# Kernel optimization log

Measured on AMD Instinct MI355X. Metric: run time of the kernel, lower is better.

Reference implementation:

```python
import jax, jax.numpy as jnp
import numpy as np

BN_EPS = 1e-5


def grid_sample_bilinear(img, grid):
    """Torch F.grid_sample, mode=bilinear, padding_mode=zeros, align_corners=False.
    img: (B, C, H, W); grid: (B, N, 2) in [-1, 1] -> (B, C, N)."""
    B, C, H, W = img.shape
    x = ((grid[..., 0] + 1.0) * W - 1.0) * 0.5  # (B, N) pixel coords
    y = ((grid[..., 1] + 1.0) * H - 1.0) * 0.5
    x0 = jnp.floor(x)
    y0 = jnp.floor(y)
    x1 = x0 + 1.0
    y1 = y0 + 1.0
    wx1 = x - x0
    wx0 = 1.0 - wx1
    wy1 = y - y0
    wy0 = 1.0 - wy1
    img_flat = img.reshape(B, C, H * W)

    def corner(xi, yi, w):
        valid = (xi >= 0) & (xi <= W - 1) & (yi >= 0) & (yi <= H - 1)
        xi_c = jnp.clip(xi, 0, W - 1).astype(jnp.int32)
        yi_c = jnp.clip(yi, 0, H - 1).astype(jnp.int32)
        idx = yi_c * W + xi_c  # (B, N)
        vals = jnp.take_along_axis(img_flat, idx[:, None, :], axis=2)  # (B, C, N)
        return vals * (w * valid.astype(img.dtype))[:, None, :]

    return (corner(x0, y0, wx0 * wy0) + corner(x1, y0, wx1 * wy0)
            + corner(x0, y1, wx0 * wy1) + corner(x1, y1, wx1 * wy1))


def conv1x1(x, w, b):
    # x: (B, Cin, N), w: (Cout, Cin), b: (Cout,)
    return jnp.einsum('oi,bin->bon', w, x) + b[None, :, None]


def batchnorm1d_train(x, gamma, beta):
    # training-mode BN over (batch, length) per channel, biased variance
    mean = jnp.mean(x, axis=(0, 2), keepdims=True)
    var = jnp.mean((x - mean) ** 2, axis=(0, 2), keepdims=True)
    xn = (x - mean) * jax.lax.rsqrt(var + BN_EPS)
    return xn * gamma[None, :, None] + beta[None, :, None]


def setup_inputs() -> dict:
    key = jax.random.key(0)
    ks = jax.random.split(key, 12)
    B, N, CI, CP, H, W, R = 4, 16384, 256, 256, 64, 160, 4
    Cin = CI + CP
    Cb = CP // R

    def glorot(k, shape):
        fan_in = shape[1]
        return jax.random.normal(k, shape, dtype=jnp.float32) * (1.0 / np.sqrt(fan_in))

    return {
        'pts_img': jax.random.uniform(ks[0], (B, N, 2), dtype=jnp.float32, minval=-1.0, maxval=1.0),
        'img_feats': jax.random.normal(ks[1], (B, CI, H, W), dtype=jnp.float32),
        'pts_feats': jax.random.normal(ks[2], (B, CP, N), dtype=jnp.float32),
        'fusion_w': glorot(ks[3], (CP, Cin)),
        'fusion_b': jax.random.normal(ks[4], (CP,), dtype=jnp.float32) * 0.01,
        'bn_gamma': jnp.ones((CP,), dtype=jnp.float32),
        'bn_beta': jnp.zeros((CP,), dtype=jnp.float32),
        'ca1_w': glorot(ks[5], (Cb, CP)),
        'ca1_b': jax.random.normal(ks[6], (Cb,), dtype=jnp.float32) * 0.01,
        'ca2_w': glorot(ks[7], (CP, Cb)),
        'ca2_b': jax.random.normal(ks[8], (CP,), dtype=jnp.float32) * 0.01,
        'sa_w': glorot(ks[9], (Cb, CP)),
        'sa_b': jax.random.normal(ks[10], (Cb,), dtype=jnp.float32) * 0.01,
    }


def reference(pts_img, img_feats, pts_feats, fusion_w, fusion_b, bn_gamma, bn_beta,
              ca1_w, ca1_b, ca2_w, ca2_b, sa_w, sa_b):
    # grid_sample gather: (B, C_I, N)
    pts_wise_img_feats = grid_sample_bilinear(img_feats, pts_img)
    fusion = jnp.concatenate([pts_wise_img_feats, pts_feats], axis=1)  # (B, C_I+C_P, N)
    # fusion MLP: conv1x1 + BN + ReLU
    fusion = jax.nn.relu(batchnorm1d_train(conv1x1(fusion, fusion_w, fusion_b), bn_gamma, bn_beta))
    # spatial attention: max over channels of bottleneck conv, sigmoid gate
    spatial = jax.nn.sigmoid(jnp.max(conv1x1(fusion, sa_w, sa_b), axis=1, keepdims=True))
    fusion = spatial * fusion
    # channel attention: bottleneck MLP, global max-pool over points, sigmoid gate
    ca = conv1x1(jax.nn.relu(conv1x1(fusion, ca1_w, ca1_b)), ca2_w, ca2_b)  # (B, C_P, N)
    channel = jax.nn.sigmoid(jnp.max(ca, axis=2, keepdims=True))  # (B, C_P, 1)
    return channel * fusion
```

## Files before the change

### kernel.cpp

```cpp
#include <hip/hip_runtime.h>
#include <stdint.h>


typedef __attribute__((ext_vector_type(8))) short bf16x8;
typedef __attribute__((ext_vector_type(4))) float f32x4;

#define B_ 4
#define N_ 16384
#define H_ 64
#define W_ 160
#define HW_ (H_ * W_)
#define K_ 512

__device__ __forceinline__ float bf2f(unsigned short u) {
    union { unsigned int i; float f; } c; c.i = ((unsigned int)u) << 16; return c.f;
}
__device__ __forceinline__ unsigned short f2bf(float f) {
    union { float f; unsigned int i; } c; c.f = f;
    unsigned int u = c.i;
    return (unsigned short)((u + 0x7FFFu + ((u >> 16) & 1u)) >> 16);
}
__device__ __forceinline__ unsigned int fkey(float f) {
    union { float f; unsigned int u; int i; } c; c.f = f;
    return (c.i < 0) ? ~c.u : (c.u | 0x80000000u);
}
__device__ __forceinline__ float funkey(unsigned int k) {
    union { unsigned int u; float f; } c;
    c.u = (k & 0x80000000u) ? (k & 0x7FFFFFFFu) : ~k;
    return c.f;
}

__device__ __forceinline__ void async_copy16(void* lds, const void* g) {
#if defined(__has_builtin) && __has_builtin(__builtin_amdgcn_global_load_lds)
    __builtin_amdgcn_global_load_lds(
        (const __attribute__((address_space(1))) unsigned int*)g,
        (__attribute__((address_space(3))) unsigned int*)lds, 16, 0, 0);
#else
    *(uint4*)lds = *(const uint4*)g;
#endif
}

__global__ __launch_bounds__(256) void k_imgt(const float* __restrict__ img,
                                              unsigned short* __restrict__ imgT,
                                              const float* __restrict__ fw,
                                              const float* __restrict__ saw,
                                              const float* __restrict__ c1w,
                                              const float* __restrict__ c2w,
                                              unsigned short* WfB, unsigned short* saB,
                                              unsigned short* ca1B, unsigned short* ca2B,
                                              float* buckets, unsigned int* camax) {
    int t = threadIdx.x;
    int bx = blockIdx.x;
    if (bx < 2560) {
        __shared__ __align__(16) unsigned short tile[64 * 68];
        int hw0 = (bx % 160) * 64, c0 = ((bx / 160) & 3) * 64, b = bx / 640;
        const float* src = img + ((size_t)b * 256 + c0) * HW_ + hw0;
        int sub = (t & 15) * 4, grp = t >> 4;
#pragma unroll
        for (int it = 0; it < 4; ++it) {
            int cl = grp + it * 16;
            float4 v = *(const float4*)(src + (size_t)cl * HW_ + sub);
            ushort4 o;
            o.x = f2bf(v.x); o.y = f2bf(v.y); o.z = f2bf(v.z); o.w = f2bf(v.w);
            *(ushort4*)(tile + cl * 68 + sub) = o;
        }
        __syncthreads();
        unsigned short* dst = imgT + ((size_t)b * HW_ + hw0) * 256 + c0;
#pragma unroll
        for (int it = 0; it < 4; ++it) {
            int hwl = grp + it * 16;
            ushort4 o;
            o.x = tile[(sub + 0) * 68 + hwl];
            o.y = tile[(sub + 1) * 68 + hwl];
            o.z = tile[(sub + 2) * 68 + hwl];
            o.w = tile[(sub + 3) * 68 + hwl];
            *(ushort4*)(dst + (size_t)hwl * 256 + sub) = o;
        }
    } else {
        int j = bx - 2560;
        if (j == 0) {
            for (int i = t; i < 16 * 512; i += 256) buckets[i] = 0.f;
            for (int i = t; i < 8 * 1024; i += 256) camax[i] = 0u;
        }
        int i = j * 256 + t;
        if (i < 131072) WfB[i] = f2bf(fw[i]);
        else if (i < 147456) saB[i - 131072] = f2bf(saw[i - 131072]);
        else if (i < 163840) ca1B[i - 147456] = f2bf(c1w[i - 147456]);
        else if (i < 180224) ca2B[i - 163840] = f2bf(c2w[i - 163840]);
    }
}

__global__ __launch_bounds__(256, 3) void k_gemm1f(const unsigned short* __restrict__ WfB,
                                                   const float* __restrict__ pim,
                                                   const unsigned short* __restrict__ imgT,
                                                   const float* __restrict__ pts,
                                                   const float* __restrict__ fb,
                                                   unsigned short* __restrict__ Y,
                                                   float* __restrict__ buckets) {
    __shared__ __align__(16) char smem[47104];
    unsigned short* At = (unsigned short*)smem;
    unsigned short* Bt = (unsigned short*)(smem + 32768);
    unsigned short* tile = (unsigned short*)smem;
    uint4*  offs4 = (uint4*)(smem + 41984);
    float4* wts4  = (float4*)(smem + 43008);
    float* biasS  = (float*)(smem + 44032);
    float* redS   = (float*)(smem + 45056);
    float* redQ   = (float*)(smem + 46080);

    int t = threadIdx.x;
    int n0 = blockIdx.x * 64, bb = blockIdx.y;
    int w = t >> 6, lane = t & 63, quad = lane >> 4, l15 = lane & 15;
    const unsigned short* imb = imgT + (size_t)bb * HW_ * 256;

    if (t < 64) {
        float2 g2 = *(const float2*)(pim + (size_t)((size_t)bb * N_ + n0 + t) * 2);
        float x = (g2.x + 1.0f) * (0.5f * W_) - 0.5f;
        float y = (g2.y + 1.0f) * (0.5f * H_) - 0.5f;
        float xf = floorf(x), yf = floorf(y);
        float wx1 = x - xf, wx0 = 1.0f - wx1;
        float wy1 = y - yf, wy0 = 1.0f - wy1;
        int x0 = (int)xf, y0 = (int)yf;
        int x1 = x0 + 1, y1 = y0 + 1;
        float vx0 = (x0 >= 0 && x0 < W_) ? 1.f : 0.f;
        float vx1 = (x1 >= 0 && x1 < W_) ? 1.f : 0.f;
        float vy0 = (y0 >= 0 && y0 < H_) ? 1.f : 0.f;
        float vy1 = (y1 >= 0 && y1 < H_) ? 1.f : 0.f;
        int cx0 = min(max(x0, 0), W_ - 1), cx1 = min(max(x1, 0), W_ - 1);
        int cy0 = min(max(y0, 0), H_ - 1), cy1 = min(max(y1, 0), H_ - 1);
        uint4 o4;
        o4.x = (unsigned)(cy0 * W_ + cx0);
        o4.y = (unsigned)(cy0 * W_ + cx1);
        o4.z = (unsigned)(cy1 * W_ + cx0);
        o4.w = (unsigned)(cy1 * W_ + cx1);
        offs4[t] = o4;
        float4 w4;
        w4.x = wx0 * wy0 * vx0 * vy0;
        w4.y = wx1 * wy0 * vx1 * vy0;
        w4.z = wx0 * wy1 * vx0 * vy1;
        w4.w = wx1 * wy1 * vx1 * vy1;
        wts4[t] = w4;
    }
    biasS[t] = fb[t];

    int arow_lo = t >> 3;
    int aslot = (t & 7) ^ ((t >> 3) & 7);

    const f32x4 fzero = {0.f, 0.f, 0.f, 0.f};
    f32x4 acc[4][4];
#pragma unroll
    for (int i = 0; i < 4; ++i)
#pragma unroll
        for (int j = 0; j < 4; ++j) acc[i][j] = fzero;

    for (int kt = 0; kt < 8; ++kt) {
        int k0 = kt * 64;
        __syncthreads();
#pragma unroll
        for (int q = 0; q < 8; ++q) {
            int row = q * 32 + arow_lo;
            async_copy16(At + (size_t)q * 2048 + (size_t)t * 8,
                         WfB + (size_t)row * K_ + k0 + aslot * 8);
        }
        if (kt < 4) {
#pragma unroll
            for (int pass = 0; pass < 2; ++pass) {
                int tau = pass * 256 + t;
                int pt = tau >> 3, cg = tau & 7;
                uint4 o4 = offs4[pt];
                float4 w4 = wts4[pt];
                int ch = k0 + cg * 8;
                uint4 cA = *(const uint4*)(imb + (size_t)o4.x * 256 + ch);
                uint4 cB = *(const uint4*)(imb + (size_t)o4.y * 256 + ch);
                uint4 cC = *(const uint4*)(imb + (size_t)o4.z * 256 + ch);
                uint4 cD = *(const uint4*)(imb + (size_t)o4.w * 256 + ch);
                const unsigned short* pa = (const unsigned short*)&cA;
                const unsigned short* pb = (const unsigned short*)&cB;
                const unsigned short* pc = (const unsigned short*)&cC;
                const unsigned short* pd = (const unsigned short*)&cD;
                uint4 ov;
                unsigned short* po = (unsigned short*)&ov;
#pragma unroll
                for (int e = 0; e < 8; ++e)
                    po[e] = f2bf(w4.x * bf2f(pa[e]) + w4.y * bf2f(pb[e]) +
                                 w4.z * bf2f(pc[e]) + w4.w * bf2f(pd[e]));
                *(uint4*)(Bt + pt * 72 + cg * 8) = ov;
            }
        } else {
            int c_local = t & 63, g = t >> 6;
            int c = (kt - 4) * 64 + c_local;
            const float* src = pts + ((size_t)bb * 256 + c) * (size_t)N_ + n0 + g * 16;
            float4 v0 = *(const float4*)(src + 0);
            float4 v1 = *(const float4*)(src + 4);
            float4 v2 = *(const float4*)(src + 8);
            float4 v3 = *(const float4*)(src + 12);
            unsigned short* dst = Bt + (size_t)(g * 16) * 72 + c_local;
            dst[0 * 72] = f2bf(v0.x); dst[1 * 72] = f2bf(v0.y);
            dst[2 * 72] = f2bf(v0.z); dst[3 * 72] = f2bf(v0.w);
            dst[4 * 72] = f2bf(v1.x); dst[5 * 72] = f2bf(v1.y);
            dst[6 * 72] = f2bf(v1.z); dst[7 * 72] = f2bf(v1.w);
            dst[8 * 72] = f2bf(v2.x); dst[9 * 72] = f2bf(v2.y);
            dst[10 * 72] = f2bf(v2.z); dst[11 * 72] = f2bf(v2.w);
            dst[12 * 72] = f2bf(v3.x); dst[13 * 72] = f2bf(v3.y);
            dst[14 * 72] = f2bf(v3.z); dst[15 * 72] = f2bf(v3.w);
        }
        __syncthreads();
#pragma unroll
        for (int kk = 0; kk < 2; ++kk) {
            bf16x8 af[4], bv[4];
#pragma unroll
            for (int j = 0; j < 4; ++j)
                bv[j] = *(const bf16x8*)(Bt + (j * 16 + l15) * 72 + kk * 32 + quad * 8);
#pragma unroll
            for (int i = 0; i < 4; ++i) {
                int mloc = w * 64 + i * 16 + l15;
                int slot = (kk * 4 + quad) ^ (l15 & 7);
                af[i] = *(const bf16x8*)(At + (size_t)mloc * 64 + slot * 8);
            }
#pragma unroll
            for (int i = 0; i < 4; ++i)
#pragma unroll
                for (int j = 0; j < 4; ++j)
                    acc[i][j] = __builtin_amdgcn_mfma_f32_16x16x32_bf16(af[i], bv[j], acc[i][j], 0, 0, 0);
        }
    }

    __syncthreads();
#pragma unroll
    for (int i = 0; i < 4; ++i) {
        int mloc = w * 64 + i * 16 + quad * 4;
        float b0 = biasS[mloc + 0], b1 = biasS[mloc + 1];
        float b2 = biasS[mloc + 2], b3 = biasS[mloc + 3];
        float s0 = 0.f, q0 = 0.f, s1 = 0.f, q1 = 0.f;
        float s2 = 0.f, q2 = 0.f, s3 = 0.f, q3 = 0.f;
#pragma unroll
        for (int j = 0; j < 4; ++j) {
            int n = j * 16 + l15;
            float y0 = acc[i][j][0] + b0;
            float y1 = acc[i][j][1] + b1;
            float y2 = acc[i][j][2] + b2;
            float y3 = acc[i][j][3] + b3;
            s0 += y0; q0 += y0 * y0;
            s1 += y1; q1 += y1 * y1;
            s2 += y2; q2 += y2 * y2;
            s3 += y3; q3 += y3 * y3;
            ushort4 o;
            o.x = f2bf(y0); o.y = f2bf(y1); o.z = f2bf(y2); o.w = f2bf(y3);
            *(ushort4*)(tile + n * 264 + mloc) = o;
        }
#pragma unroll
        for (int d = 1; d < 16; d <<= 1) {
            s0 += __shfl_xor(s0, d, 64); q0 += __shfl_xor(q0, d, 64);
            s1 += __shfl_xor(s1, d, 64); q1 += __shfl_xor(q1, d, 64);
            s2 += __shfl_xor(s2, d, 64); q2 += __shfl_xor(q2, d, 64);
            s3 += __shfl_xor(s3, d, 64); q3 += __shfl_xor(q3, d, 64);
        }
        if (l15 == 0) {
            redS[mloc + 0] = s0; redQ[mloc + 0] = q0;
            redS[mloc + 1] = s1; redQ[mloc + 1] = q1;
            redS[mloc + 2] = s2; redQ[mloc + 2] = q2;
            redS[mloc + 3] = s3; redQ[mloc + 3] = q3;
        }
    }
    __syncthreads();
    {
        float* bk = buckets + (size_t)(blockIdx.x & 15) * 512;
        atomicAdd(bk + t, redS[t]);
        atomicAdd(bk + 256 + t, redQ[t]);
    }
    size_t Yrow0 = ((size_t)bb * N_ + n0) * 256;
#pragma unroll
    for (int pass = 0; pass < 8; ++pass) {
        int row = pass * 8 + (t >> 5);
        int col = (t & 31) * 8;
        *(uint4*)(Y + Yrow0 + (size_t)row * 256 + col) = *(const uint4*)(tile + row * 264 + col);
    }
}

__global__ __launch_bounds__(256, 2) void k_gate(const unsigned short* __restrict__ Y,
                                                 const float* __restrict__ buckets,
                                                 const float* __restrict__ gamma,
                                                 const float* __restrict__ beta,
                                                 const unsigned short* __restrict__ saB,
                                                 const float* __restrict__ sab,
                                                 const unsigned short* __restrict__ c1B,
                                                 const float* __restrict__ c1b,
                                                 const unsigned short* __restrict__ c2B,
                                                 unsigned int* __restrict__ camax,
                                                 float* __restrict__ sp_g,
                                                 float* __restrict__ ss_out) {
    __shared__ __align__(16) unsigned short Ft[64 * 264];
    __shared__ __align__(16) unsigned short Ht[64 * 72];
    __shared__ float scS[256], shS[256];
    __shared__ float saPart[4][64];
    __shared__ float spL[64];
    int t = threadIdx.x;
    size_t pts0 = (size_t)blockIdx.x * 64;
    int b = (int)(pts0 >> 14);
    int w = t >> 6, lane = t & 63, quad = lane >> 4, l15 = lane & 15;
    int jrow = w * 16 + l15;

    bf16x8 bvs[8], bvc[8];
#pragma unroll
    for (int kt = 0; kt < 8; ++kt) {
        bvs[kt] = *(const bf16x8*)(saB + (size_t)jrow * 256 + kt * 32 + quad * 8);
        bvc[kt] = *(const bf16x8*)(c1B + (size_t)jrow * 256 + kt * 32 + quad * 8);
    }
    float sbias = sab[jrow];
    float cbias = c1b[jrow];

    {
        float s = 0.f, q = 0.f;
#pragma unroll
        for (int bk = 0; bk < 16; ++bk) {
            s += buckets[bk * 512 + t];
            q += buckets[bk * 512 + 256 + t];
        }
        const float inv = 1.0f / (float)(B_ * N_);
        float mean = s * inv;
        float var = q * inv - mean * mean;
        float sc = gamma[t] * rsqrtf(var + 1e-5f);
        float sh = beta[t] - mean * sc;
        scS[t] = sc;
        shS[t] = sh;
        if (blockIdx.x == 0) { ss_out[t] = sc; ss_out[256 + t] = sh; }
    }
    __syncthreads();

    int cc = (t * 8) & 255;
    float scr[8], shr[8];
#pragma unroll
    for (int e = 0; e < 8; ++e) { scr[e] = scS[cc + e]; shr[e] = shS[cc + e]; }
    for (int idx = t * 8; idx < 64 * 256; idx += 2048) {
        int r = idx >> 8;
        uint4 v = *(const uint4*)(Y + (pts0 + r) * 256 + cc);
        unsigned short* us = (unsigned short*)&v;
#pragma unroll
        for (int e = 0; e < 8; ++e) {
            float f = bf2f(us[e]) * scr[e] + shr[e];
            us[e] = f2bf(fmaxf(f, 0.f));
        }
        *(uint4*)(Ft + r * 264 + cc) = v;
    }
    __syncthreads();

    const f32x4 fzero = {0.f, 0.f, 0.f, 0.f};
    f32x4 accS[4], accC[4];
#pragma unroll
    for (int i = 0; i < 4; ++i) { accS[i] = fzero; accC[i] = fzero; }
#pragma unroll
    for (int kt = 0; kt < 8; ++kt) {
        bf16x8 af[4];
#pragma unroll
        for (int i = 0; i < 4; ++i)
            af[i] = *(const bf16x8*)(Ft + (i * 16 + l15) * 264 + kt * 32 + quad * 8);
#pragma unroll
        for (int i = 0; i < 4; ++i) {
            accS[i] = __builtin_amdgcn_mfma_f32_16x16x32_bf16(af[i], bvs[kt], accS[i], 0, 0, 0);
            accC[i] = __builtin_amdgcn_mfma_f32_16x16x32_bf16(af[i], bvc[kt], accC[i], 0, 0, 0);
        }
    }
#pragma unroll
    for (int i = 0; i < 4; ++i) {
#pragma unroll
        for (int r = 0; r < 4; ++r) {
            float v = accS[i][r] + sbias;
#pragma unroll
            for (int d = 1; d < 16; d <<= 1) v = fmaxf(v, __shfl_xor(v, d, 64));
            if (l15 == 0) saPart[w][i * 16 + quad * 4 + r] = v;
        }
    }
    __syncthreads();
    if (t < 64) {
        float m4 = fmaxf(fmaxf(saPart[0][t], saPart[1][t]),
                         fmaxf(saPart[2][t], saPart[3][t]));
        float sv = 1.0f / (1.0f + __expf(-m4));
        spL[t] = sv;
        sp_g[pts0 + t] = sv;
    }
    __syncthreads();

#pragma unroll
    for (int i = 0; i < 4; ++i) {
#pragma unroll
        for (int r = 0; r < 4; ++r) {
            int pt = i * 16 + quad * 4 + r;
            float hv = fmaxf(accC[i][r] * spL[pt] + cbias, 0.f);
            Ht[pt * 72 + jrow] = f2bf(hv);
        }
    }
    __syncthreads();

    {
        bf16x8 b2a[4], b2b[4];
#pragma unroll
        for (int mt = 0; mt < 4; ++mt) {
            b2a[mt] = *(const bf16x8*)(c2B + (size_t)(w * 64 + mt * 16 + l15) * 64 + quad * 8);
            b2b[mt] = *(const bf16x8*)(c2B + (size_t)(w * 64 + mt * 16 + l15) * 64 + 32 + quad * 8);
        }
        float vmax[4] = {-3e38f, -3e38f, -3e38f, -3e38f};
#pragma unroll
        for (int i = 0; i < 4; ++i) {
            bf16x8 a0 = *(const bf16x8*)(Ht + (i * 16 + l15) * 72 + quad * 8);
            bf16x8 a1 = *(const bf16x8*)(Ht + (i * 16 + l15) * 72 + 32 + quad * 8);
#pragma unroll
            for (int mt = 0; mt < 4; ++mt) {
                f32x4 acc = __builtin_amdgcn_mfma_f32_16x16x32_bf16(a0, b2a[mt], fzero, 0, 0, 0);
                acc = __builtin_amdgcn_mfma_f32_16x16x32_bf16(a1, b2b[mt], acc, 0, 0, 0);
#pragma unroll
                for (int r = 0; r < 4; ++r) vmax[mt] = fmaxf(vmax[mt], acc[r]);
            }
        }
        unsigned int* cam = camax + (size_t)(blockIdx.x & 7) * 1024 + b * 256;
#pragma unroll
        for (int mt = 0; mt < 4; ++mt) {
            float v = vmax[mt];
            v = fmaxf(v, __shfl_xor(v, 16, 64));
            v = fmaxf(v, __shfl_xor(v, 32, 64));
            if (quad == 0) atomicMax(cam + w * 64 + mt * 16 + l15, fkey(v));
        }
    }
}

__global__ __launch_bounds__(256) void k_out(const unsigned short* __restrict__ Y,
                                             const unsigned int* __restrict__ camax,
                                             const float* __restrict__ c2b,
                                             const float* __restrict__ ss,
                                             const float* __restrict__ sp_g,
                                             float* __restrict__ out) {
    __shared__ __align__(16) unsigned short tile[64 * 68];
    __shared__ float ch[64], scT[64], shT[64], spT[64];
    int t = threadIdx.x;
    int n0 = blockIdx.x * 64, m0 = blockIdx.y * 64, b = blockIdx.z;
    if (t < 64) {
        int m = m0 + t;
        unsigned int k = 0u;
#pragma unroll
        for (int bk = 0; bk < 8; ++bk) k = max(k, camax[bk * 1024 + b * 256 + m]);
        ch[t] = 1.0f / (1.0f + __expf(-(funkey(k) + c2b[m])));
        scT[t] = ss[m];
        shT[t] = ss[256 + m];
        spT[t] = sp_g[(size_t)b * N_ + n0 + t];
    }
    int sub = (t & 15) * 4, grp = t >> 4;
    const unsigned short* src = Y + ((size_t)b * N_ + n0) * 256 + m0;
#pragma unroll
    for (int it = 0; it < 4; ++it) {
        int nl = grp + it * 16;
        ushort4 v = *(const ushort4*)(src + (size_t)nl * 256 + sub);
        *(ushort4*)(tile + nl * 68 + sub) = v;
    }
    __syncthreads();
    float* dst = out + ((size_t)b * 256 + m0) * N_ + n0;
#pragma unroll
    for (int it = 0; it < 4; ++it) {
        int ml = grp + it * 16;
        float g = ch[ml], scv = scT[ml], shv = shT[ml];
        float4 o;
        o.x = fmaxf(bf2f(tile[(sub + 0) * 68 + ml]) * scv + shv, 0.f) * spT[sub + 0] * g;
        o.y = fmaxf(bf2f(tile[(sub + 1) * 68 + ml]) * scv + shv, 0.f) * spT[sub + 1] * g;
        o.z = fmaxf(bf2f(tile[(sub + 2) * 68 + ml]) * scv + shv, 0.f) * spT[sub + 2] * g;
        o.w = fmaxf(bf2f(tile[(sub + 3) * 68 + ml]) * scv + shv, 0.f) * spT[sub + 3] * g;
        *(float4*)(dst + (size_t)ml * N_ + sub) = o;
    }
}

extern "C" void kernel_launch(void* const* d_in, const int* in_sizes, int n_in,
                              void* d_out, int out_size, void* d_ws, size_t ws_size,
                              hipStream_t stream) {
    (void)in_sizes; (void)n_in; (void)out_size; (void)ws_size;
    const float* pts_img = (const float*)d_in[0];
    const float* img     = (const float*)d_in[1];
    const float* pts     = (const float*)d_in[2];
    const float* fw      = (const float*)d_in[3];
    const float* fbias   = (const float*)d_in[4];
    const float* gamma   = (const float*)d_in[5];
    const float* beta    = (const float*)d_in[6];
    const float* c1w     = (const float*)d_in[7];
    const float* c1b     = (const float*)d_in[8];
    const float* c2w     = (const float*)d_in[9];
    const float* c2b     = (const float*)d_in[10];
    const float* saw     = (const float*)d_in[11];
    const float* sab     = (const float*)d_in[12];
    float* out = (float*)d_out;

    char* ws = (char*)d_ws;
    unsigned short* imgT = (unsigned short*)(ws);
    unsigned short* Y    = (unsigned short*)(ws + 20971520);
    unsigned short* WfB  = (unsigned short*)(ws + 54525952);
    unsigned short* saB  = (unsigned short*)(ws + 54788096);
    unsigned short* ca1B = (unsigned short*)(ws + 54820864);
    unsigned short* ca2B = (unsigned short*)(ws + 54853632);
    float* buckets       = (float*)(ws + 54886400);
    unsigned int* camax  = (unsigned int*)(ws + 54919168);
    float* sp_g          = (float*)(ws + 54951936);
    float* ss            = (float*)(ws + 55214080);

    k_imgt<<<3264, 256, 0, stream>>>(img, imgT, fw, saw, c1w, c2w,
                                     WfB, saB, ca1B, ca2B, buckets, camax);
    k_gemm1f<<<dim3(256, 4), 256, 0, stream>>>(WfB, pts_img, imgT, pts, fbias, Y, buckets);
    k_gate<<<1024, 256, 0, stream>>>(Y, buckets, gamma, beta, saB, sab, ca1B, c1b,
                                     ca2B, camax, sp_g, ss);
    k_out<<<dim3(256, 4, 4), 256, 0, stream>>>(Y, camax, c2b, ss, sp_g, out);
}
```

Baseline: 250.0 us.

## Widen k_out tiles to all channels, interleave gemm1 batches, raise gate occupancy

k_out now has each block load a full 64-point by 256-channel Y tile with 16-byte row-contiguous reads and write all 256 channels, replacing 64x64 sub-tiles. The scale, shift and channel-gate setup therefore runs once per block rather than once per channel group, and the grid shrinks from 4096 to 1024 blocks. k_gemm1f switches to a 1D grid with the batch index in the low bits, so consecutive blocks cover different batches and spread their gathers and atomic buckets. k_gate's launch bounds go from 2 to 3 blocks per SM, which may force register spills. The larger k_out tile uses about 35KB of LDS, which limits how many blocks can be resident per CU.

```diff
diff --git a/kernel.cpp b/kernel.cpp
--- a/kernel.cpp
+++ b/kernel.cpp
@@ -108,7 +108,9 @@
     float* redQ   = (float*)(smem + 46080);
 
     int t = threadIdx.x;
-    int n0 = blockIdx.x * 64, bb = blockIdx.y;
+    int bid = blockIdx.x;
+    int bb = bid & 3;
+    int n0 = (bid >> 2) * 64;
     int w = t >> 6, lane = t & 63, quad = lane >> 4, l15 = lane & 15;
     const unsigned short* imb = imgT + (size_t)bb * HW_ * 256;
 
@@ -263,7 +265,7 @@
     }
     __syncthreads();
     {
-        float* bk = buckets + (size_t)(blockIdx.x & 15) * 512;
+        float* bk = buckets + (size_t)(bid & 15) * 512;
         atomicAdd(bk + t, redS[t]);
         atomicAdd(bk + 256 + t, redQ[t]);
     }
@@ -276,7 +278,7 @@
     }
 }
 
-__global__ __launch_bounds__(256, 2) void k_gate(const unsigned short* __restrict__ Y,
+__global__ __launch_bounds__(256, 3) void k_gate(const unsigned short* __restrict__ Y,
                                                  const float* __restrict__ buckets,
                                                  const float* __restrict__ gamma,
                                                  const float* __restrict__ beta,
@@ -427,40 +429,40 @@
                                              const float* __restrict__ ss,
                                              const float* __restrict__ sp_g,
                                              float* __restrict__ out) {
-    __shared__ __align__(16) unsigned short tile[64 * 68];
-    __shared__ float ch[64], scT[64], shT[64], spT[64];
+    __shared__ __align__(16) unsigned short tile[64 * 264];
+    __shared__ float ch[256], scT[256], shT[256], spT[64];
     int t = threadIdx.x;
-    int n0 = blockIdx.x * 64, m0 = blockIdx.y * 64, b = blockIdx.z;
-    if (t < 64) {
-        int m = m0 + t;
+    int n0 = blockIdx.x * 64, b = blockIdx.y;
+    {
+        int m = t;
         unsigned int k = 0u;
 #pragma unroll
         for (int bk = 0; bk < 8; ++bk) k = max(k, camax[bk * 1024 + b * 256 + m]);
         ch[t] = 1.0f / (1.0f + __expf(-(funkey(k) + c2b[m])));
         scT[t] = ss[m];
         shT[t] = ss[256 + m];
-        spT[t] = sp_g[(size_t)b * N_ + n0 + t];
-    }
+    }
+    if (t < 64) spT[t] = sp_g[(size_t)b * N_ + n0 + t];
+    const unsigned short* src = Y + ((size_t)b * N_ + n0) * 256;
+#pragma unroll
+    for (int pass = 0; pass < 8; ++pass) {
+        int row = pass * 8 + (t >> 5);
+        int col = (t & 31) * 8;
+        *(uint4*)(tile + row * 264 + col) = *(const uint4*)(src + (size_t)row * 256 + col);
+    }
+    __syncthreads();
     int sub = (t & 15) * 4, grp = t >> 4;
-    const unsigned short* src = Y + ((size_t)b * N_ + n0) * 256 + m0;
-#pragma unroll
-    for (int it = 0; it < 4; ++it) {
-        int nl = grp + it * 16;
-        ushort4 v = *(const ushort4*)(src + (size_t)nl * 256 + sub);
-        *(ushort4*)(tile + nl * 68 + sub) = v;
-    }
-    __syncthreads();
-    float* dst = out + ((size_t)b * 256 + m0) * N_ + n0;
-#pragma unroll
-    for (int it = 0; it < 4; ++it) {
+#pragma unroll
+    for (int it = 0; it < 16; ++it) {
         int ml = grp + it * 16;
         float g = ch[ml], scv = scT[ml], shv = shT[ml];
+        float* dst = out + ((size_t)b * 256 + ml) * N_ + n0;
         float4 o;
-        o.x = fmaxf(bf2f(tile[(sub + 0) * 68 + ml]) * scv + shv, 0.f) * spT[sub + 0] * g;
-        o.y = fmaxf(bf2f(tile[(sub + 1) * 68 + ml]) * scv + shv, 0.f) * spT[sub + 1] * g;
-        o.z = fmaxf(bf2f(tile[(sub + 2) * 68 + ml]) * scv + shv, 0.f) * spT[sub + 2] * g;
-        o.w = fmaxf(bf2f(tile[(sub + 3) * 68 + ml]) * scv + shv, 0.f) * spT[sub + 3] * g;
-        *(float4*)(dst + (size_t)ml * N_ + sub) = o;
+        o.x = fmaxf(bf2f(tile[(sub + 0) * 264 + ml]) * scv + shv, 0.f) * spT[sub + 0] * g;
+        o.y = fmaxf(bf2f(tile[(sub + 1) * 264 + ml]) * scv + shv, 0.f) * spT[sub + 1] * g;
+        o.z = fmaxf(bf2f(tile[(sub + 2) * 264 + ml]) * scv + shv, 0.f) * spT[sub + 2] * g;
+        o.w = fmaxf(bf2f(tile[(sub + 3) * 264 + ml]) * scv + shv, 0.f) * spT[sub + 3] * g;
+        *(float4*)(dst + sub) = o;
     }
 }
 
@@ -497,8 +499,8 @@
 
     k_imgt<<<3264, 256, 0, stream>>>(img, imgT, fw, saw, c1w, c2w,
                                      WfB, saB, ca1B, ca2B, buckets, camax);
-    k_gemm1f<<<dim3(256, 4), 256, 0, stream>>>(WfB, pts_img, imgT, pts, fbias, Y, buckets);
+    k_gemm1f<<<1024, 256, 0, stream>>>(WfB, pts_img, imgT, pts, fbias, Y, buckets);
     k_gate<<<1024, 256, 0, stream>>>(Y, buckets, gamma, beta, saB, sab, ca1B, c1b,
                                      ca2B, camax, sp_g, ss);
-    k_out<<<dim3(256, 4, 4), 256, 0, stream>>>(Y, camax, c2b, ss, sp_g, out);
-}
+    k_out<<<dim3(256, 4), 256, 0, stream>>>(Y, camax, c2b, ss, sp_g, out);
+}
```

Measured after the change: 250.5 us. Within noise of the previous version (+0.2%).
